# Optimization experiments

Measured on AMD Instinct MI355X. Metric: run time of the kernel, lower is better.

## Reference

```python
import jax, jax.numpy as jnp
import numpy as np

SPH, SPW = 24, 24          # spatial tile size
NBLK = 2                   # channel blocks (in_channels // 512)
EPS = 1e-5


def _tiles(h, w):
    nh = int(np.ceil(h / SPH)); nw = int(np.ceil(w / SPW))
    sh = (h - SPH) // (nh - 1) if nh > 1 else 0
    sw = (w - SPW) // (nw - 1) if nw > 1 else 0
    offs = []
    for i in range(nh):
        for j in range(nw):
            offs.append((max(0, i * sh), max(0, j * sw)))
    return offs, nh, nw


def _mlp(x_v, w1, b1, w2, b2):
    # 1x1 conv1d pair over the spatial_area axis: x_v (B, S, C)
    h = jax.nn.relu(jnp.einsum('os,bsc->boc', w1, x_v) + b1[None, :, None])
    return jnp.einsum('so,boc->bsc', w2, h) + b2[None, :, None]


def _forward(x, w_in1, b_in1, w_in2, b_in2, w_out1, b_out1, w_out2, b_out2, bn_gamma, bn_beta):
    bt, c, h, w = x.shape
    offs, nh, nw = _tiles(h, w)
    # gather overlapping (here exactly tiling) spatial patches -> stacked chunk batch
    chunks = [x[:, :, ty:ty + SPH, tx:tx + SPW].reshape(bt, c, SPH * SPW) for ty, tx in offs]
    x_stacked = jnp.concatenate(chunks, 0)            # (nchunks*bt, c, S)
    x_v = jnp.transpose(x_stacked, (0, 2, 1))         # (B, S, c)
    x_v = _mlp(x_v, w_in1, b_in1, w_in2, b_in2)
    # negative squared-distance score over channel means (no detach in this branch)
    x_m = x_v.mean(axis=1)                            # (B, c)
    score = -(x_m[:, None, :] - x_m[:, :, None]) ** 2  # (B, c, c)
    blk = c // NBLK
    ids = jnp.arange(c) // blk
    mask = ids[:, None] == ids[None, :]               # block-diagonal channel mask
    score = jnp.where(mask[None], score, -jnp.inf)
    attn = jax.nn.softmax(score, axis=1)              # softmax over dim 1 (rows)
    out = jnp.einsum('bsc,bcd->bsd', x_v, attn)       # torch.bmm(x_v, attn)
    out = _mlp(out, w_out1, b_out1, w_out2, b_out2)
    # BatchNorm1d(spatial_area) in training mode: stats over (B, c) per S-channel
    mu = out.mean(axis=(0, 2), keepdims=True)
    var = out.var(axis=(0, 2), keepdims=True)
    out = (out - mu) * jax.lax.rsqrt(var + EPS) * bn_gamma[None, :, None] + bn_beta[None, :, None]
    out = jnp.transpose(out, (0, 2, 1))               # (B, c, S)
    # scatter_add chunks back (scaled by 1/spblock_h^2, as in the original)
    scale = 1.0 / (nh * nh)
    res = x
    for idx, (ty, tx) in enumerate(offs):
        chunk = out[idx * bt:(idx + 1) * bt].reshape(bt, c, SPH, SPW)
        res = res.at[:, :, ty:ty + SPH, tx:tx + SPW].add(chunk * scale)
    return jax.nn.relu(res)


def setup_inputs() -> dict:
    key = jax.random.key(0)
    ks = jax.random.split(key, 9)
    S = SPH * SPW          # 576
    H = S // 8             # 72 (reduction=8)
    s = 0.02
    return {
        'x': jax.random.normal(ks[0], (16, 1024, 48, 48), dtype=jnp.float32),
        'w_in1': jax.random.normal(ks[1], (H, S), dtype=jnp.float32) * s,
        'b_in1': jnp.zeros((H,), jnp.float32),
        'w_in2': jax.random.normal(ks[2], (S, H), dtype=jnp.float32) * s,
        'b_in2': jnp.zeros((S,), jnp.float32),
        'w_out1': jax.random.normal(ks[3], (H, S), dtype=jnp.float32) * s,
        'b_out1': jnp.zeros((H,), jnp.float32),
        'w_out2': jax.random.normal(ks[4], (S, H), dtype=jnp.float32) * s,
        'b_out2': jnp.zeros((S,), jnp.float32),
        'bn_gamma': jnp.ones((S,), jnp.float32),
        'bn_beta': jnp.zeros((S,), jnp.float32),
    }


def reference(x, w_in1, b_in1, w_in2, b_in2, w_out1, b_out1, w_out2, b_out2, bn_gamma, bn_beta):
    return _forward(x, w_in1, b_in1, w_in2, b_in2, w_out1, b_out1, w_out2, b_out2, bn_gamma, bn_beta)
```

## Files before the change

### kernel.cpp

```cpp
#include <hip/hip_runtime.h>
#include <hip/hip_bf16.h>


#define EPS 1e-5f

typedef __attribute__((ext_vector_type(8))) short short8;
typedef __attribute__((ext_vector_type(4))) short short4v;
typedef __attribute__((ext_vector_type(4))) float f32x4;
typedef __attribute__((ext_vector_type(4))) float float4v;

#define GLD_LDS(g, l) __builtin_amdgcn_global_load_lds( \
    (const __attribute__((address_space(1))) void*)(g), \
    (__attribute__((address_space(3))) void*)(l), 16, 0, 0)

static __device__ __forceinline__ unsigned short f2bu(float f) {
    union { __hip_bfloat16 h; unsigned short u; } cv;
    cv.h = __float2bfloat16(f);
    return cv.u;
}

__global__ void prep_k(const float* __restrict__ w_in1, const float* __restrict__ b_in1,
                       const float* __restrict__ w_in2,
                       const float* __restrict__ w_out1, const float* __restrict__ b_out1,
                       const float* __restrict__ w_out2,
                       __hip_bfloat16* __restrict__ w1p, __hip_bfloat16* __restrict__ w2p,
                       __hip_bfloat16* __restrict__ w2op, __hip_bfloat16* __restrict__ w1oq,
                       float* __restrict__ b1p, float* __restrict__ b1op)
{
    int i = blockIdx.x * 256 + threadIdx.x;
    if (i < 128 * 576) {
        int r = i / 576, c = i - r * 576;
        w1p[i] = __float2bfloat16(r < 72 ? w_in1[r * 576 + c] : 0.f);
    }
    if (i < 640 * 96) {
        int r = i / 96, c = i - r * 96;
        bool ok = (r < 576) && (c < 72);
        w2p[i]  = __float2bfloat16(ok ? w_in2[r * 72 + c] : 0.f);
        w2op[i] = __float2bfloat16(ok ? w_out2[r * 72 + c] : 0.f);
    }
    if (i < 128 * 640) {
        int r = i / 640, c = i - r * 640;
        w1oq[i] = __float2bfloat16((r < 72 && c < 576) ? w_out1[r * 576 + c] : 0.f);
    }
    if (i < 128) {
        b1p[i]  = i < 72 ? b_in1[i] : 0.f;
        b1op[i] = i < 72 ? b_out1[i] : 0.f;
    }
}

__global__ void extract_k(const float4v* __restrict__ x4, __hip_bfloat16* __restrict__ xv)
{
    int i = blockIdx.x * 256 + threadIdx.x;
    int s4 = i % 144;
    int m = i / 144;
    int c = m & 1023;
    int b = m >> 10;
    int n = b & 15, ti = b >> 4;
    int ty = (ti >> 1) * 24, tx = (ti & 1) * 24;
    int s = s4 * 4;
    int sy = s / 24, sx = s - sy * 24;
    float4v v = x4[((((n << 10) + c) * 48 + ty + sy) * 48 + tx + sx) >> 2];
    short4v pk;
    pk.x = (short)f2bu(v.x); pk.y = (short)f2bu(v.y);
    pk.z = (short)f2bu(v.z); pk.w = (short)f2bu(v.w);
    *(short4v*)(xv + (long)i * 4) = pk;
}

__global__ __launch_bounds__(256) void fused_mlp1G(
    const unsigned short* __restrict__ A,
    const unsigned short* __restrict__ W1,
    const float* __restrict__ b1,
    const unsigned short* __restrict__ W2,
    const float* __restrict__ b2,
    const unsigned short* __restrict__ W1O,
    unsigned short* __restrict__ G,
    float* __restrict__ xm_raw)
{
    __shared__ __align__(16) unsigned short smem[4096 + 4096 + 13312 + 17408];
    unsigned short* As = smem;
    unsigned short* Bs = smem + 4096;
    unsigned short* Hs = smem + 8192;
    unsigned short* T  = smem + 21504;

    const int m0 = blockIdx.x * 128;
    const int t = threadIdx.x;
    const int lane = t & 63, wave = t >> 6;
    const int wr = wave >> 1, wc = wave & 1;
    const int lrow = lane & 15, kq = (lane >> 4) * 8;
    const int cr = (lane >> 4) * 4;
    const int r0 = t >> 2, c0 = (t & 3) * 8;

    f32x4 acc[4][4];
    #pragma unroll
    for (int i = 0; i < 4; ++i)
        #pragma unroll
        for (int j = 0; j < 4; ++j)
            acc[i][j] = (f32x4){0.f, 0.f, 0.f, 0.f};

    for (int k0 = 0; k0 < 576; k0 += 32) {
        GLD_LDS(A + (long)(m0 + r0) * 576 + k0 + c0,      &As[t * 8]);
        GLD_LDS(A + (long)(m0 + r0 + 64) * 576 + k0 + c0, &As[(t + 256) * 8]);
        GLD_LDS(W1 + (long)r0 * 576 + k0 + c0,            &Bs[t * 8]);
        GLD_LDS(W1 + (long)(r0 + 64) * 576 + k0 + c0,     &Bs[(t + 256) * 8]);
        __syncthreads();
        short8 af[4], bf[4];
        #pragma unroll
        for (int i = 0; i < 4; ++i)
            af[i] = *(const short8*)&As[(wr * 64 + i * 16 + lrow) * 32 + kq];
        #pragma unroll
        for (int j = 0; j < 4; ++j)
            bf[j] = *(const short8*)&Bs[(wc * 64 + j * 16 + lrow) * 32 + kq];
        #pragma unroll
        for (int i = 0; i < 4; ++i)
            #pragma unroll
            for (int j = 0; j < 4; ++j)
                acc[i][j] = __builtin_amdgcn_mfma_f32_16x16x32_bf16(af[i], bf[j], acc[i][j], 0, 0, 0);
        __syncthreads();
    }

    #pragma unroll
    for (int j = 0; j < 4; ++j) {
        int col = wc * 64 + j * 16 + lrow;
        if (col < 96) {
            float bv = b1[col];
            #pragma unroll
            for (int i = 0; i < 4; ++i) {
                int row = wr * 64 + i * 16 + cr;
                #pragma unroll
                for (int r = 0; r < 4; ++r)
                    Hs[(row + r) * 104 + col] = f2bu(fmaxf(acc[i][j][r] + bv, 0.f));
            }
        }
    }
    __syncthreads();

    float rsum[4][4];
    #pragma unroll
    for (int i = 0; i < 4; ++i)
        #pragma unroll
        for (int r = 0; r < 4; ++r)
            rsum[i][r] = 0.f;

    f32x4 gacc[4][4];
    #pragma unroll
    for (int i = 0; i < 4; ++i)
        #pragma unroll
        for (int j = 0; j < 4; ++j)
            gacc[i][j] = (f32x4){0.f, 0.f, 0.f, 0.f};

    const int z = m0 >> 9, m_local = m0 & 511;

    for (int n0 = 0; n0 < 640; n0 += 128) {
        f32x4 a2[4][4];
        #pragma unroll
        for (int i = 0; i < 4; ++i)
            #pragma unroll
            for (int j = 0; j < 4; ++j)
                a2[i][j] = (f32x4){0.f, 0.f, 0.f, 0.f};

        for (int k0 = 0; k0 < 96; k0 += 32) {
            GLD_LDS(W2 + (long)(n0 + r0) * 96 + k0 + c0,      &Bs[t * 8]);
            GLD_LDS(W2 + (long)(n0 + r0 + 64) * 96 + k0 + c0, &Bs[(t + 256) * 8]);
            __syncthreads();
            short8 af[4], bf[4];
            #pragma unroll
            for (int i = 0; i < 4; ++i)
                af[i] = *(const short8*)&Hs[(wr * 64 + i * 16 + lrow) * 104 + k0 + kq];
            #pragma unroll
            for (int j = 0; j < 4; ++j)
                bf[j] = *(const short8*)&Bs[(wc * 64 + j * 16 + lrow) * 32 + kq];
            #pragma unroll
            for (int i = 0; i < 4; ++i)
                #pragma unroll
                for (int j = 0; j < 4; ++j)
                    a2[i][j] = __builtin_amdgcn_mfma_f32_16x16x32_bf16(af[i], bf[j], a2[i][j], 0, 0, 0);
            __syncthreads();
        }

        #pragma unroll
        for (int i = 0; i < 4; ++i)
            #pragma unroll
            for (int r = 0; r < 4; ++r)
                rsum[i][r] += a2[i][0][r] + a2[i][1][r] + a2[i][2][r] + a2[i][3][r];

        #pragma unroll
        for (int j = 0; j < 4; ++j) {
            int col = wc * 64 + j * 16 + lrow;
            float bv = (n0 + col < 576) ? b2[n0 + col] : 0.f;
            #pragma unroll
            for (int i = 0; i < 4; ++i) {
                int row = wr * 64 + i * 16 + cr;
                #pragma unroll
                for (int r = 0; r < 4; ++r)
                    T[(row + r) * 136 + col] = f2bu(a2[i][j][r] + bv);
            }
        }
        __syncthreads();

        for (int kk = 0; kk < 128; kk += 32) {
            GLD_LDS(W1O + (long)r0 * 640 + n0 + kk + c0,        &As[t * 8]);
            GLD_LDS(W1O + (long)(r0 + 64) * 640 + n0 + kk + c0, &As[(t + 256) * 8]);
            __syncthreads();
            short8 af[4], bf[4];
            #pragma unroll
            for (int i = 0; i < 4; ++i)
                af[i] = *(const short8*)&As[(wr * 64 + i * 16 + lrow) * 32 + kq];
            #pragma unroll
            for (int j = 0; j < 4; ++j)
                bf[j] = *(const short8*)&T[(wc * 64 + j * 16 + lrow) * 136 + kk + kq];
            #pragma unroll
            for (int i = 0; i < 4; ++i)
                #pragma unroll
                for (int j = 0; j < 4; ++j)
                    gacc[i][j] = __builtin_amdgcn_mfma_f32_16x16x32_bf16(af[i], bf[j], gacc[i][j], 0, 0, 0);
            __syncthreads();
        }
    }

    #pragma unroll
    for (int i = 0; i < 4; ++i)
        #pragma unroll
        for (int r = 0; r < 4; ++r) {
            float v = rsum[i][r];
            v += __shfl_xor(v, 1, 64);
            v += __shfl_xor(v, 2, 64);
            v += __shfl_xor(v, 4, 64);
            v += __shfl_xor(v, 8, 64);
            if (lrow == 0)
                atomicAdd(&xm_raw[m0 + wr * 64 + i * 16 + cr + r], v);
        }

    unsigned short* Gz = G + (long)z * 128 * 512;
    #pragma unroll
    for (int j = 0; j < 4; ++j) {
        int cn = wc * 64 + j * 16 + lrow;
        #pragma unroll
        for (int i = 0; i < 4; ++i) {
            int h = wr * 64 + i * 16 + cr;
            #pragma unroll
            for (int r = 0; r < 4; ++r)
                Gz[(long)(h + r) * 512 + m_local + cn] = f2bu(gacc[i][j][r]);
        }
    }
}

__global__ void denom_k(const float* __restrict__ xm_raw, const float* __restrict__ b_in2,
                        float* __restrict__ xmn, float* __restrict__ invd)
{
    __shared__ float sx[512];
    __shared__ float red[256];
    int z = blockIdx.x;
    int t = threadIdx.x;
    float p = 0.f;
    for (int i = t; i < 576; i += 256) p += b_in2[i];
    red[t] = p; __syncthreads();
    for (int o = 128; o; o >>= 1) { if (t < o) red[t] += red[t + o]; __syncthreads(); }
    float btot = red[0];
    for (int i = t; i < 512; i += 256) {
        float m = (xm_raw[(long)z * 512 + i] + btot) * (1.f / 576.f);
        sx[i] = m;
        xmn[(long)z * 512 + i] = m;
    }
    __syncthreads();
    #pragma unroll
    for (int dd = 0; dd < 2; ++dd) {
        int d = t + dd * 256;
        float xd = sx[d], s = 0.f;
        for (int c = 0; c < 512; ++c) { float df = sx[c] - xd; s += __expf(-df * df); }
        invd[(long)z * 512 + d] = 1.f / s;
    }
}

__global__ __launch_bounds__(256) void fused_attn_mlp2(
    const unsigned short* __restrict__ G,
    const float* __restrict__ xmn, const float* __restrict__ invd,
    const float* __restrict__ b1,
    const unsigned short* __restrict__ W2,
    const float* __restrict__ b2,
    __hip_bfloat16* __restrict__ C,
    float* __restrict__ statsR)
{
    __shared__ __align__(16) unsigned short smem[4096 + 4096 + 13312];
    unsigned short* As = smem;
    unsigned short* Bs = smem + 4096;
    unsigned short* Hs = smem + 8192;
    __shared__ float sxm[512];
    __shared__ float sinv[128];

    int bid = blockIdx.x;
    int lb = (bid & 7) * 64 + (bid >> 3);
    int z = lb >> 2;
    const int m0 = (lb & 3) * 128;
    const int t = threadIdx.x;
    const int lane = t & 63, wave = t >> 6;
    const int wr = wave >> 1, wc = wave & 1;
    const int lrow = lane & 15, kq = (lane >> 4) * 8;
    const int cr = (lane >> 4) * 4;
    const int r0 = t >> 2, c0 = (t & 3) * 8;
    const unsigned short* Gz = G + (long)z * 128 * 512;

    for (int i = t; i < 512; i += 256) sxm[i] = xmn[(long)z * 512 + i];
    if (t < 128) sinv[t] = invd[(long)z * 512 + m0 + t];
    __syncthreads();

    const int dA = t >> 1, cbA = (t & 1) * 16;
    const float xd = sxm[m0 + dA];
    const float ivd = sinv[dA];

    f32x4 acc[4][4];
    #pragma unroll
    for (int i = 0; i < 4; ++i)
        #pragma unroll
        for (int j = 0; j < 4; ++j)
            acc[i][j] = (f32x4){0.f, 0.f, 0.f, 0.f};

    for (int k0 = 0; k0 < 512; k0 += 32) {
        GLD_LDS(Gz + (long)r0 * 512 + k0 + c0,        &Bs[t * 8]);
        GLD_LDS(Gz + (long)(r0 + 64) * 512 + k0 + c0, &Bs[(t + 256) * 8]);
        short8 pk0, pk1;
        #pragma unroll
        for (int e = 0; e < 8; ++e) {
            float d0 = sxm[k0 + cbA + e] - xd;
            pk0[e] = (short)f2bu(__expf(-d0 * d0) * ivd);
            float d1 = sxm[k0 + cbA + 8 + e] - xd;
            pk1[e] = (short)f2bu(__expf(-d1 * d1) * ivd);
        }
        *(short8*)&As[dA * 32 + cbA]     = pk0;
        *(short8*)&As[dA * 32 + cbA + 8] = pk1;
        __syncthreads();
        short8 af[4], bf[4];
        #pragma unroll
        for (int i = 0; i < 4; ++i)
            af[i] = *(const short8*)&As[(wr * 64 + i * 16 + lrow) * 32 + kq];
        #pragma unroll
        for (int j = 0; j < 4; ++j)
            bf[j] = *(const short8*)&Bs[(wc * 64 + j * 16 + lrow) * 32 + kq];
        #pragma unroll
        for (int i = 0; i < 4; ++i)
            #pragma unroll
            for (int j = 0; j < 4; ++j)
                acc[i][j] = __builtin_amdgcn_mfma_f32_16x16x32_bf16(af[i], bf[j], acc[i][j], 0, 0, 0);
        __syncthreads();
    }

    #pragma unroll
    for (int j = 0; j < 4; ++j) {
        int col = wc * 64 + j * 16 + lrow;
        if (col < 96) {
            float bv = b1[col];
            #pragma unroll
            for (int i = 0; i < 4; ++i) {
                int row = wr * 64 + i * 16 + cr;
                #pragma unroll
                for (int r = 0; r < 4; ++r)
                    Hs[(row + r) * 104 + col] = f2bu(fmaxf(acc[i][j][r] + bv, 0.f));
            }
        }
    }
    __syncthreads();

    const long mg = (long)z * 512 + m0;
    float* st = statsR + (bid & 7) * 1152;
    for (int n0 = 0; n0 < 640; n0 += 128) {
        f32x4 a2[4][4];
        #pragma unroll
        for (int i = 0; i < 4; ++i)
            #pragma unroll
            for (int j = 0; j < 4; ++j)
                a2[i][j] = (f32x4){0.f, 0.f, 0.f, 0.f};

        for (int k0 = 0; k0 < 96; k0 += 32) {
            GLD_LDS(W2 + (long)(n0 + r0) * 96 + k0 + c0,      &Bs[t * 8]);
            GLD_LDS(W2 + (long)(n0 + r0 + 64) * 96 + k0 + c0, &Bs[(t + 256) * 8]);
            __syncthreads();
            short8 af[4], bf[4];
            #pragma unroll
            for (int i = 0; i < 4; ++i)
                af[i] = *(const short8*)&Hs[(wr * 64 + i * 16 + lrow) * 104 + k0 + kq];
            #pragma unroll
            for (int j = 0; j < 4; ++j)
                bf[j] = *(const short8*)&Bs[(wc * 64 + j * 16 + lrow) * 32 + kq];
            #pragma unroll
            for (int i = 0; i < 4; ++i)
                #pragma unroll
                for (int j = 0; j < 4; ++j)
                    a2[i][j] = __builtin_amdgcn_mfma_f32_16x16x32_bf16(af[i], bf[j], a2[i][j], 0, 0, 0);
            __syncthreads();
        }

        #pragma unroll
        for (int j = 0; j < 4; ++j) {
            int col = n0 + wc * 64 + j * 16 + lrow;
            bool live = col < 576;
            float bv = live ? b2[col] : 0.f;
            float s1 = 0.f, s2 = 0.f;
            #pragma unroll
            for (int i = 0; i < 4; ++i) {
                long rowb = (mg + wr * 64 + i * 16 + cr) * 576;
                #pragma unroll
                for (int r = 0; r < 4; ++r) {
                    float v = a2[i][j][r] + bv;
                    s1 += v; s2 += v * v;
                    if (live) C[rowb + (long)r * 576 + col] = __float2bfloat16(v);
                }
            }
            s1 += __shfl_xor(s1, 16, 64); s1 += __shfl_xor(s1, 32, 64);
            s2 += __shfl_xor(s2, 16, 64); s2 += __shfl_xor(s2, 32, 64);
            if ((lane >> 4) == 0 && live) {
                atomicAdd(&st[col], s1);
                atomicAdd(&st[576 + col], s2);
            }
        }
    }
}

__global__ void bnfin_k(const float* __restrict__ statsR,
                        const float* __restrict__ gamma, const float* __restrict__ beta,
                        float* __restrict__ ab)
{
    int s = threadIdx.x;
    float sum = 0.f, sq = 0.f;
    #pragma unroll
    for (int r = 0; r < 8; ++r) {
        sum += statsR[r * 1152 + s];
        sq  += statsR[r * 1152 + 576 + s];
    }
    float mu = sum * (1.f / 65536.f);
    float var = sq * (1.f / 65536.f) - mu * mu;
    float a = gamma[s] * rsqrtf(var + EPS);
    ab[s] = a;
    ab[576 + s] = beta[s] - mu * a;
}

__global__ void final_k(const float4v* __restrict__ x4, const __hip_bfloat16* __restrict__ out3,
                        const float* __restrict__ ab, float4v* __restrict__ out4)
{
    int i = blockIdx.x * 256 + threadIdx.x;
    int xx4 = i % 12; int t = i / 12;
    int y = t % 48; t /= 48;
    int c = t & 1023; int n = t >> 10;
    int xx = xx4 * 4;
    int ti = (y / 24) * 2 + (xx / 24);
    int b = ti * 16 + n;
    int s = (y % 24) * 24 + (xx % 24);
    const __hip_bfloat16* o3 = out3 + (((long)b << 10) + c) * 576 + s;
    float4v xv = x4[i];
    float4v o;
    #pragma unroll
    for (int e = 0; e < 4; ++e) {
        float v = __bfloat162float(o3[e]);
        float bn = v * ab[s + e] + ab[576 + s + e];
        float r = (e == 0 ? xv.x : e == 1 ? xv.y : e == 2 ? xv.z : xv.w) + 0.25f * bn;
        if (e == 0) o.x = fmaxf(r, 0.f);
        else if (e == 1) o.y = fmaxf(r, 0.f);
        else if (e == 2) o.z = fmaxf(r, 0.f);
        else o.w = fmaxf(r, 0.f);
    }
    out4[i] = o;
}

extern "C" void kernel_launch(void* const* d_in, const int* in_sizes, int n_in,
                              void* d_out, int out_size, void* d_ws, size_t ws_size,
                              hipStream_t stream)
{
    const float* x      = (const float*)d_in[0];
    const float* w_in1  = (const float*)d_in[1];
    const float* b_in1  = (const float*)d_in[2];
    const float* w_in2  = (const float*)d_in[3];
    const float* b_in2  = (const float*)d_in[4];
    const float* w_out1 = (const float*)d_in[5];
    const float* b_out1 = (const float*)d_in[6];
    const float* w_out2 = (const float*)d_in[7];
    const float* b_out2 = (const float*)d_in[8];
    const float* gamma  = (const float*)d_in[9];
    const float* beta   = (const float*)d_in[10];

    char* ws = (char*)d_ws;
    __hip_bfloat16* xv0    = (__hip_bfloat16*)(ws);
    __hip_bfloat16* out3   = (__hip_bfloat16*)(ws + 75497472L);
    unsigned short* G      = (unsigned short*)(ws + 150994944L);
    float*          xmn    = (float*)(ws + 167772160L);
    float*          xm_raw = (float*)(ws + 168034304L);
    float*          invd   = (float*)(ws + 168296448L);
    float*          statsR = (float*)(ws + 168558592L);
    float*          ab     = (float*)(ws + 168595456L);
    __hip_bfloat16* w1p    = (__hip_bfloat16*)(ws + 168600064L);
    __hip_bfloat16* w2p    = (__hip_bfloat16*)(ws + 168747520L);
    __hip_bfloat16* w2op   = (__hip_bfloat16*)(ws + 168870400L);
    __hip_bfloat16* w1oq   = (__hip_bfloat16*)(ws + 168993280L);
    float*          b1p    = (float*)(ws + 169157120L);
    float*          b1op   = (float*)(ws + 169157632L);

    hipMemsetAsync(xm_raw, 0, 262144, stream);
    hipMemsetAsync(statsR, 0, 36864, stream);

    prep_k<<<320, 256, 0, stream>>>(w_in1, b_in1, w_in2, w_out1, b_out1, w_out2,
                                    w1p, w2p, w2op, w1oq, b1p, b1op);

    extract_k<<<36864, 256, 0, stream>>>((const float4v*)x, xv0);

    fused_mlp1G<<<512, 256, 0, stream>>>(
        (const unsigned short*)xv0, (const unsigned short*)w1p, b1p,
        (const unsigned short*)w2p, b_in2, (const unsigned short*)w1oq,
        G, xm_raw);

    denom_k<<<128, 256, 0, stream>>>(xm_raw, b_in2, xmn, invd);

    fused_attn_mlp2<<<512, 256, 0, stream>>>(
        G, xmn, invd, b1op, (const unsigned short*)w2op, b_out2,
        out3, statsR);

    bnfin_k<<<1, 576, 0, stream>>>(statsR, gamma, beta, ab);

    final_k<<<36864, 256, 0, stream>>>((const float4v*)x, out3, ab, (float4v*)d_out);
}
```

Before: 517.2 us.

## Precompose w_out1·w_in2 into a single 72x72 matrix, skipping the 576-wide intermediate

Since attention mixes channels while the MLP layers mix the spatial axis, w_out1·w_in2 can be folded into one small matrix computed once by a new prep kernel. The folded bias is passed to the second stage. An extra row of column sums of w_in2 yields the channel mean directly, which removes the atomics and the memset. This drops the per-block 576-wide second GEMM and the third GEMM in favour of one K=96 GEMM, so there is much less MFMA and LDS work. In exchange the product is rounded to bf16 once more, and the prep kernel runs serial 576-long dot products.

```diff
diff --git a/kernel.cpp b/kernel.cpp
--- a/kernel.cpp
+++ b/kernel.cpp
@@ -20,12 +20,9 @@
 }
 
 __global__ void prep_k(const float* __restrict__ w_in1, const float* __restrict__ b_in1,
-                       const float* __restrict__ w_in2,
-                       const float* __restrict__ w_out1, const float* __restrict__ b_out1,
-                       const float* __restrict__ w_out2,
-                       __hip_bfloat16* __restrict__ w1p, __hip_bfloat16* __restrict__ w2p,
-                       __hip_bfloat16* __restrict__ w2op, __hip_bfloat16* __restrict__ w1oq,
-                       float* __restrict__ b1p, float* __restrict__ b1op)
+                       const float* __restrict__ w_in2, const float* __restrict__ w_out2,
+                       __hip_bfloat16* __restrict__ w1p, __hip_bfloat16* __restrict__ w2op,
+                       float* __restrict__ b1p)
 {
     int i = blockIdx.x * 256 + threadIdx.x;
     if (i < 128 * 576) {
@@ -35,16 +32,34 @@
     if (i < 640 * 96) {
         int r = i / 96, c = i - r * 96;
         bool ok = (r < 576) && (c < 72);
-        w2p[i]  = __float2bfloat16(ok ? w_in2[r * 72 + c] : 0.f);
         w2op[i] = __float2bfloat16(ok ? w_out2[r * 72 + c] : 0.f);
     }
-    if (i < 128 * 640) {
-        int r = i / 640, c = i - r * 640;
-        w1oq[i] = __float2bfloat16((r < 72 && c < 576) ? w_out1[r * 576 + c] : 0.f);
-    }
-    if (i < 128) {
-        b1p[i]  = i < 72 ? b_in1[i] : 0.f;
-        b1op[i] = i < 72 ? b_out1[i] : 0.f;
+    if (i < 128)
+        b1p[i] = i < 72 ? b_in1[i] : 0.f;
+}
+
+__global__ void prepM_k(const float* __restrict__ w_out1, const float* __restrict__ w_in2,
+                        const float* __restrict__ b_in2, const float* __restrict__ b_out1,
+                        __hip_bfloat16* __restrict__ Mp, float* __restrict__ b1G)
+{
+    int i = blockIdx.x * 256 + threadIdx.x;
+    if (i >= 128 * 96) return;
+    int h = i / 96, k = i - h * 96;
+    float m = 0.f;
+    if (h < 72 && k < 72) {
+        for (int s = 0; s < 576; ++s)
+            m += w_out1[h * 576 + s] * w_in2[s * 72 + k];
+    } else if (h == 72 && k < 72) {
+        for (int s = 0; s < 576; ++s)
+            m += w_in2[s * 72 + k];
+    }
+    Mp[i] = __float2bfloat16(m);
+    if (k == 0) {
+        float c = 0.f;
+        if (h < 72)
+            for (int s = 0; s < 576; ++s)
+                c += w_out1[h * 576 + s] * b_in2[s];
+        b1G[h] = (h < 72) ? b_out1[h] + c : 0.f;
     }
 }
 
@@ -66,21 +81,18 @@
     *(short4v*)(xv + (long)i * 4) = pk;
 }
 
-__global__ __launch_bounds__(256) void fused_mlp1G(
+__global__ __launch_bounds__(256) void fused_mlp1(
     const unsigned short* __restrict__ A,
     const unsigned short* __restrict__ W1,
     const float* __restrict__ b1,
-    const unsigned short* __restrict__ W2,
-    const float* __restrict__ b2,
-    const unsigned short* __restrict__ W1O,
+    const unsigned short* __restrict__ Mp,
     unsigned short* __restrict__ G,
     float* __restrict__ xm_raw)
 {
-    __shared__ __align__(16) unsigned short smem[4096 + 4096 + 13312 + 17408];
+    __shared__ __align__(16) unsigned short smem[4096 + 4096 + 13312];
     unsigned short* As = smem;
     unsigned short* Bs = smem + 4096;
     unsigned short* Hs = smem + 8192;
-    unsigned short* T  = smem + 21504;
 
     const int m0 = blockIdx.x * 128;
     const int t = threadIdx.x;
@@ -134,103 +146,35 @@
     }
     __syncthreads();
 
-    float rsum[4][4];
+    f32x4 gacc[4][4];
     #pragma unroll
     for (int i = 0; i < 4; ++i)
         #pragma unroll
-        for (int r = 0; r < 4; ++r)
-            rsum[i][r] = 0.f;
-
-    f32x4 gacc[4][4];
-    #pragma unroll
-    for (int i = 0; i < 4; ++i)
-        #pragma unroll
         for (int j = 0; j < 4; ++j)
             gacc[i][j] = (f32x4){0.f, 0.f, 0.f, 0.f};
 
+    for (int k0 = 0; k0 < 96; k0 += 32) {
+        GLD_LDS(Mp + (long)r0 * 96 + k0 + c0,        &As[t * 8]);
+        GLD_LDS(Mp + (long)(r0 + 64) * 96 + k0 + c0, &As[(t + 256) * 8]);
+        __syncthreads();
+        short8 af[4], bf[4];
+        #pragma unroll
+        for (int i = 0; i < 4; ++i)
+            af[i] = *(const short8*)&As[(wr * 64 + i * 16 + lrow) * 32 + kq];
+        #pragma unroll
+        for (int j = 0; j < 4; ++j)
+            bf[j] = *(const short8*)&Hs[(wc * 64 + j * 16 + lrow) * 104 + k0 + kq];
+        #pragma unroll
+        for (int i = 0; i < 4; ++i)
+            #pragma unroll
+            for (int j = 0; j < 4; ++j)
+                gacc[i][j] = __builtin_amdgcn_mfma_f32_16x16x32_bf16(af[i], bf[j], gacc[i][j], 0, 0, 0);
+        __syncthreads();
+    }
+
     const int z = m0 >> 9, m_local = m0 & 511;
-
-    for (int n0 = 0; n0 < 640; n0 += 128) {
-        f32x4 a2[4][4];
-        #pragma unroll
-        for (int i = 0; i < 4; ++i)
-            #pragma unroll
-            for (int j = 0; j < 4; ++j)
-                a2[i][j] = (f32x4){0.f, 0.f, 0.f, 0.f};
-
-        for (int k0 = 0; k0 < 96; k0 += 32) {
-            GLD_LDS(W2 + (long)(n0 + r0) * 96 + k0 + c0,      &Bs[t * 8]);
-            GLD_LDS(W2 + (long)(n0 + r0 + 64) * 96 + k0 + c0, &Bs[(t + 256) * 8]);
-            __syncthreads();
-            short8 af[4], bf[4];
-            #pragma unroll
-            for (int i = 0; i < 4; ++i)
-                af[i] = *(const short8*)&Hs[(wr * 64 + i * 16 + lrow) * 104 + k0 + kq];
-            #pragma unroll
-            for (int j = 0; j < 4; ++j)
-                bf[j] = *(const short8*)&Bs[(wc * 64 + j * 16 + lrow) * 32 + kq];
-            #pragma unroll
-            for (int i = 0; i < 4; ++i)
-                #pragma unroll
-                for (int j = 0; j < 4; ++j)
-                    a2[i][j] = __builtin_amdgcn_mfma_f32_16x16x32_bf16(af[i], bf[j], a2[i][j], 0, 0, 0);
-            __syncthreads();
-        }
-
-        #pragma unroll
-        for (int i = 0; i < 4; ++i)
-            #pragma unroll
-            for (int r = 0; r < 4; ++r)
-                rsum[i][r] += a2[i][0][r] + a2[i][1][r] + a2[i][2][r] + a2[i][3][r];
-
-        #pragma unroll
-        for (int j = 0; j < 4; ++j) {
-            int col = wc * 64 + j * 16 + lrow;
-            float bv = (n0 + col < 576) ? b2[n0 + col] : 0.f;
-            #pragma unroll
-            for (int i = 0; i < 4; ++i) {
-                int row = wr * 64 + i * 16 + cr;
-                #pragma unroll
-                for (int r = 0; r < 4; ++r)
-                    T[(row + r) * 136 + col] = f2bu(a2[i][j][r] + bv);
-            }
-        }
-        __syncthreads();
-
-        for (int kk = 0; kk < 128; kk += 32) {
-            GLD_LDS(W1O + (long)r0 * 640 + n0 + kk + c0,        &As[t * 8]);
-            GLD_LDS(W1O + (long)(r0 + 64) * 640 + n0 + kk + c0, &As[(t + 256) * 8]);
-            __syncthreads();
-            short8 af[4], bf[4];
-            #pragma unroll
-            for (int i = 0; i < 4; ++i)
-                af[i] = *(const short8*)&As[(wr * 64 + i * 16 + lrow) * 32 + kq];
-            #pragma unroll
-            for (int j = 0; j < 4; ++j)
-                bf[j] = *(const short8*)&T[(wc * 64 + j * 16 + lrow) * 136 + kk + kq];
-            #pragma unroll
-            for (int i = 0; i < 4; ++i)
-                #pragma unroll
-                for (int j = 0; j < 4; ++j)
-                    gacc[i][j] = __builtin_amdgcn_mfma_f32_16x16x32_bf16(af[i], bf[j], gacc[i][j], 0, 0, 0);
-            __syncthreads();
-        }
-    }
-
-    #pragma unroll
-    for (int i = 0; i < 4; ++i)
-        #pragma unroll
-        for (int r = 0; r < 4; ++r) {
-            float v = rsum[i][r];
-            v += __shfl_xor(v, 1, 64);
-            v += __shfl_xor(v, 2, 64);
-            v += __shfl_xor(v, 4, 64);
-            v += __shfl_xor(v, 8, 64);
-            if (lrow == 0)
-                atomicAdd(&xm_raw[m0 + wr * 64 + i * 16 + cr + r], v);
-        }
-
     unsigned short* Gz = G + (long)z * 128 * 512;
+
     #pragma unroll
     for (int j = 0; j < 4; ++j) {
         int cn = wc * 64 + j * 16 + lrow;
@@ -241,6 +185,12 @@
             for (int r = 0; r < 4; ++r)
                 Gz[(long)(h + r) * 512 + m_local + cn] = f2bu(gacc[i][j][r]);
         }
+    }
+
+    if (wr == 1 && cr == 8) {
+        #pragma unroll
+        for (int j = 0; j < 4; ++j)
+            xm_raw[(long)z * 512 + m_local + wc * 64 + j * 16 + lrow] = gacc[0][j][0];
     }
 }
 
@@ -485,29 +435,26 @@
     float*          statsR = (float*)(ws + 168558592L);
     float*          ab     = (float*)(ws + 168595456L);
     __hip_bfloat16* w1p    = (__hip_bfloat16*)(ws + 168600064L);
-    __hip_bfloat16* w2p    = (__hip_bfloat16*)(ws + 168747520L);
-    __hip_bfloat16* w2op   = (__hip_bfloat16*)(ws + 168870400L);
-    __hip_bfloat16* w1oq   = (__hip_bfloat16*)(ws + 168993280L);
-    float*          b1p    = (float*)(ws + 169157120L);
-    float*          b1op   = (float*)(ws + 169157632L);
-
-    hipMemsetAsync(xm_raw, 0, 262144, stream);
+    __hip_bfloat16* w2op   = (__hip_bfloat16*)(ws + 168747520L);
+    float*          b1p    = (float*)(ws + 168870400L);
+    __hip_bfloat16* Mp     = (__hip_bfloat16*)(ws + 168870912L);
+    float*          b1G    = (float*)(ws + 168895488L);
+
     hipMemsetAsync(statsR, 0, 36864, stream);
 
-    prep_k<<<320, 256, 0, stream>>>(w_in1, b_in1, w_in2, w_out1, b_out1, w_out2,
-                                    w1p, w2p, w2op, w1oq, b1p, b1op);
+    prep_k<<<288, 256, 0, stream>>>(w_in1, b_in1, w_in2, w_out2, w1p, w2op, b1p);
+    prepM_k<<<48, 256, 0, stream>>>(w_out1, w_in2, b_in2, b_out1, Mp, b1G);
 
     extract_k<<<36864, 256, 0, stream>>>((const float4v*)x, xv0);
 
-    fused_mlp1G<<<512, 256, 0, stream>>>(
+    fused_mlp1<<<512, 256, 0, stream>>>(
         (const unsigned short*)xv0, (const unsigned short*)w1p, b1p,
-        (const unsigned short*)w2p, b_in2, (const unsigned short*)w1oq,
-        G, xm_raw);
+        (const unsigned short*)Mp, G, xm_raw);
 
     denom_k<<<128, 256, 0, stream>>>(xm_raw, b_in2, xmn, invd);
 
     fused_attn_mlp2<<<512, 256, 0, stream>>>(
-        G, xmn, invd, b1op, (const unsigned short*)w2op, b_out2,
+        G, xmn, invd, b1G, (const unsigned short*)w2op, b_out2,
         out3, statsR);
 
     bnfin_k<<<1, 576, 0, stream>>>(statsR, gamma, beta, ab);
```

Measured after the change: 484.7 us. 6.3% less time.
